# Kernel optimization log

Hardware: AMD Instinct MI355X
Metric: run time of the kernel (lower is better)

The kernel has to match this reference:

```python
import jax, jax.numpy as jnp
import numpy as np

WD = WH = WW = 7      # cubic window
NH = 3                # num_heads
RATE = 1              # idx == 1 -> rate = 1, num_heads_rate = 0
FF = 3.0              # focusing_factor (<= 6 branch)
EPS = 1e-6


def setup_inputs() -> dict:
    key = jax.random.key(0)
    ks = jax.random.split(key, 6)
    B, D, H, W, C = 1, 56, 56, 56, 96
    hd = C // NH
    x = jax.random.normal(ks[0], (B, D, H, W, C), dtype=jnp.float32)
    w_qkv = jax.random.normal(ks[1], (C, 3 * C), dtype=jnp.float32) * 0.02
    scale_param = jnp.zeros((RATE, 1, 1, hd), dtype=jnp.float32)
    pos_enc = jax.random.normal(ks[2], (RATE, 1, WD * WH * WW, hd), dtype=jnp.float32) * 0.02
    dwc_w = jax.random.normal(ks[3], (hd * RATE, 1, 5, 5, 5), dtype=jnp.float32) * 0.02
    dwc_b = jnp.zeros((hd * RATE,), dtype=jnp.float32)
    w_proj = jax.random.normal(ks[4], (C, C), dtype=jnp.float32) * 0.02
    b_proj = jnp.zeros((C,), dtype=jnp.float32)
    return {"x": x, "w_qkv": w_qkv, "scale_param": scale_param, "pos_enc": pos_enc,
            "dwc_w": dwc_w, "dwc_b": dwc_b, "w_proj": w_proj, "b_proj": b_proj}


def _forward(x, w_qkv, scale_param, pos_enc, dwc_w, dwc_b, w_proj, b_proj):
    B, D, H, W, C = x.shape
    hd = C // NH
    nD, nH_, nW_ = D // WD, H // WH, W // WW
    N = WD * WH * WW
    # qkv projection (no bias) -> (3, B, D, H, W, C)
    qkv = (x @ w_qkv).reshape(B, D, H, W, 3, C).transpose(4, 0, 1, 2, 3, 5)
    # window partition (rate == 1): (3, 1, B*nWin, N, C)
    qkv = qkv.reshape(3, B, nD, WD, nH_, WH, nW_, WW, C)
    qkv = qkv.transpose(0, 1, 2, 4, 6, 3, 5, 7, 8).reshape(3, RATE, B * nD * nH_ * nW_, N, C)
    q, k, v = qkv[0], qkv[1], qkv[2]

    def heads(t):  # 'r b n (h c) -> r (b h) n c'
        r, b, n, c0 = t.shape
        return t.reshape(r, b, n, NH, hd).transpose(0, 1, 3, 2, 4).reshape(r, b * NH, n, hd)

    q, k, v = heads(q), heads(k), heads(v)
    k = k + pos_enc
    scale = jax.nn.softplus(scale_param)
    q = (jax.nn.relu(q) + EPS) / scale
    k = (jax.nn.relu(k) + EPS) / scale
    qn = jnp.linalg.norm(q, axis=-1, keepdims=True)
    kn = jnp.linalg.norm(k, axis=-1, keepdims=True)
    q = q ** FF
    k = k ** FF
    q = q / jnp.linalg.norm(q, axis=-1, keepdims=True) * qn
    k = k / jnp.linalg.norm(k, axis=-1, keepdims=True) * kn
    # linear attention, kv-first branch (i*j*(c+d) > c*d*(i+j) for N=343, hd=32)
    z = 1.0 / (jnp.einsum('rbic,rbc->rbi', q, k.sum(axis=2)) + EPS)
    kv = jnp.einsum('rbjc,rbjd->rbcd', k, v)
    out = jnp.einsum('rbic,rbcd,rbi->rbid', q, kv, z)
    # depthwise 3D conv feature map on v: 'r b (d w h) c -> b (r c) d w h'
    r, b, n, c = v.shape
    fm = v.reshape(r, b, WD, WH, WW, c).transpose(1, 0, 5, 2, 3, 4).reshape(b, r * c, WD, WH, WW)
    fm = jax.lax.conv_general_dilated(fm, dwc_w, (1, 1, 1), [(2, 2)] * 3,
                                      dimension_numbers=('NCDHW', 'OIDHW', 'NCDHW'),
                                      feature_group_count=r * c)
    fm = fm + dwc_b[None, :, None, None, None]
    fm = fm.reshape(b, r, c, WD, WH, WW).transpose(1, 0, 3, 4, 5, 2).reshape(r, b, n, c)
    out = out + fm
    # merge heads: 'r (b h) n c -> r b n (h c)'
    Bw = b // NH
    out = out.reshape(r, Bw, NH, n, hd).transpose(0, 1, 3, 2, 4).reshape(r, Bw, n, C)
    # window reverse (rate == 1)
    out = out.reshape(B, nD, nH_, nW_, WD, WH, WW, C)
    out = out.transpose(0, 1, 4, 2, 5, 3, 6, 7).reshape(B, D, H, W, C)
    return out @ w_proj + b_proj


def reference(x, w_qkv, scale_param, pos_enc, dwc_w, dwc_b, w_proj, b_proj):
    return _forward(x, w_qkv, scale_param, pos_enc, dwc_w, dwc_b, w_proj, b_proj)
```

## Files before the change

### kernel.cpp

```cpp
#include <hip/hip_runtime.h>
#include <math.h>

#define NWIN 512
#define NHD  3
#define NTOK 343
#define HD   32
#define CH   96
#define DIM  56

#define XS 16.0f
#define WS 1024.0f
#define RS (1.0f/16384.0f)

typedef __attribute__((ext_vector_type(8))) _Float16 f16x8;
typedef __attribute__((ext_vector_type(4))) float f32x4;
typedef __attribute__((ext_vector_type(2))) _Float16 h2;

__device__ __forceinline__ unsigned short f2h_bits(float x) {
    _Float16 h = (_Float16)x;
    return __builtin_bit_cast(unsigned short, h);
}
__device__ __forceinline__ float h2f_bits(unsigned short u) {
    return (float)__builtin_bit_cast(_Float16, u);
}
__device__ __forceinline__ f32x4 mfma16h(f16x8 a, f16x8 b, f32x4 c) {
    return __builtin_amdgcn_mfma_f32_16x16x32_f16(a, b, c, 0, 0, 0);
}
__device__ __forceinline__ float shfl16_sum(float v) {
    v += __shfl_xor(v, 1);
    v += __shfl_xor(v, 2);
    v += __shfl_xor(v, 4);
    v += __shfl_xor(v, 8);
    return v;
}

__global__ void setup_w(const float* __restrict__ w_qkv,
                        unsigned short* __restrict__ wsb)
{
    int i = blockIdx.x * 256 + threadIdx.x;
    if (i >= 108 * 512) return;
    int e = i & 7, l = (i >> 3) & 63;
    int fid = i >> 9;
    int hl = fid & 1; int f2 = fid >> 1;
    int ks = f2 % 3; int f3 = f2 / 3;
    int nt = f3 & 1; int f4 = f3 >> 1;
    int m  = f4 % 3; int h  = f4 / 3;
    int kg  = ks * 32 + (l >> 4) * 8 + e;
    int col = m * 96 + h * 32 + nt * 16 + (l & 15);
    float w = w_qkv[kg * 288 + col] * WS;
    unsigned short hi = f2h_bits(w);
    wsb[i] = hl ? f2h_bits(w - h2f_bits(hi)) : hi;
}

#define BUILD_AFRAG(AH, AL, XPTR)                                           \
  { _Pragma("unroll")                                                       \
    for (int ks = 0; ks < 3; ++ks) {                                        \
        float4 x0 = *(const float4*)((XPTR) + ks * 32);                     \
        float4 x1 = *(const float4*)((XPTR) + ks * 32 + 4);                 \
        union { _Float16 e[8]; f16x8 v; } th, tl;                           \
        float s[8] = {x0.x, x0.y, x0.z, x0.w, x1.x, x1.y, x1.z, x1.w};      \
        _Pragma("unroll")                                                   \
        for (int e = 0; e < 8; ++e) {                                       \
            float sv = s[e] * XS;                                           \
            unsigned short hi = f2h_bits(sv);                               \
            th.e[e] = __builtin_bit_cast(_Float16, hi);                     \
            tl.e[e] = (_Float16)(sv - h2f_bits(hi));                       \
        }                                                                   \
        AH[ks] = th.v; AL[ks] = tl.v;                                       \
    } }

__global__ __launch_bounds__(256, 4) void attn_kernel(
    const float* __restrict__ x, const unsigned short* __restrict__ wsb,
    const float* __restrict__ scale_param, const float* __restrict__ pos_enc,
    const float* __restrict__ dwc_w, const float* __restrict__ dwc_b,
    float* __restrict__ y)
{
    __shared__ __align__(16) unsigned short v16[352 * HD];
    __shared__ __align__(16) union UU {
        struct PA { unsigned short kf16c[64 * 34]; } pa;
        struct PB {
            unsigned short qfL[64 * 40];
            unsigned short kvS[32 * 40];
            float ksred[4][2][16];
        } pb;
        unsigned dwcP[16 * 125];
        float pad_pin_lds[4000];
    } u;
    __shared__ float ksum_s[HD];
    __shared__ float sps[HD];

    const int tid = threadIdx.x, bid = blockIdx.x;
    const int swz = (bid & 7) * 192 + (bid >> 3);
    const int win = swz / 3;
    const int h   = swz - win * 3;
    const int wd = win >> 6, wh = (win >> 3) & 7, ww = win & 7;
    const int wv = tid >> 6, lane = tid & 63;
    const int quad = lane >> 4, li = lane & 15;
    const int mtw = wv >> 1, ntw = wv & 1;

    if (tid < HD) {
        float sv = scale_param[tid];
        sps[tid] = (sv > 20.f) ? sv : log1pf(expf(sv));
    }
    __syncthreads();
    const float sp0 = sps[li], sp1 = sps[16 + li];

    const f16x8* wf = (const f16x8*)wsb;
    const int fbase = h * 36;
    float ksp0 = 0.f, ksp1 = 0.f;
    f32x4 kvacc = {0.f, 0.f, 0.f, 0.f};

    for (int cb0 = 0; cb0 < NTOK; cb0 += 64) {
        const int nj = min(64, NTOK - cb0);
        int atok = cb0 + wv * 16 + li;
        int atc = min(atok, NTOK - 1);
        int adz = atc / 49, arem = atc - adz * 49, ady = arem / 7, adx = arem - ady * 7;
        int gA = ((wd * 7 + adz) * DIM + (wh * 7 + ady)) * DIM + (ww * 7 + adx);
        const float* xr = x + (size_t)gA * CH + quad * 8;
        f16x8 ah[3], al[3];
        BUILD_AFRAG(ah, al, xr);

        f32x4 ak[2] = {{0,0,0,0},{0,0,0,0}};
        f32x4 av[2] = {{0,0,0,0},{0,0,0,0}};
        #pragma unroll
        for (int nt = 0; nt < 2; ++nt) {
            #pragma unroll
            for (int ks = 0; ks < 3; ++ks) {
                int fk = (fbase + ((1 * 2 + nt) * 3 + ks) * 2) * 64 + lane;
                int fv = (fbase + ((2 * 2 + nt) * 3 + ks) * 2) * 64 + lane;
                f16x8 bkh = wf[fk], bkl = wf[fk + 64];
                f16x8 bvh = wf[fv];
                ak[nt] = mfma16h(ah[ks], bkh, ak[nt]);
                ak[nt] = mfma16h(ah[ks], bkl, ak[nt]);
                ak[nt] = mfma16h(al[ks], bkh, ak[nt]);
                av[nt] = mfma16h(ah[ks], bvh, av[nt]);
                av[nt] = mfma16h(al[ks], bvh, av[nt]);
            }
        }

        #pragma unroll
        for (int j = 0; j < 4; ++j) {
            int t16 = quad * 4 + j;
            int tok = cb0 + wv * 16 + t16;
            bool val = tok < NTOK;
            int tc = val ? tok : NTOK - 1;
            float pe0 = pos_enc[tc * HD + li];
            float pe1 = pos_enc[tc * HD + 16 + li];
            float kr0 = ak[0][j] * RS + pe0;
            float kr1 = ak[1][j] * RS + pe1;
            float kp0 = (fmaxf(kr0, 0.f) + 1e-6f) / sp0;
            float kp1 = (fmaxf(kr1, 0.f) + 1e-6f) / sp1;
            float k30 = kp0 * kp0 * kp0, k31 = kp1 * kp1 * kp1;
            float n2k = fmaf(kp0, kp0, kp1 * kp1);
            float n6k = fmaf(k30, k30, k31 * k31);
            n2k = shfl16_sum(n2k); n6k = shfl16_sum(n6k);
            float sk = sqrtf(n2k / n6k);
            float kf0 = k30 * sk, kf1 = k31 * sk;
            int tl = wv * 16 + t16;
            if (val) {
                ksp0 += kf0; ksp1 += kf1;
                u.pa.kf16c[tl * 34 + li]      = f2h_bits(kf0);
                u.pa.kf16c[tl * 34 + 16 + li] = f2h_bits(kf1);
                v16[tok * HD + li]      = f2h_bits(av[0][j] * RS);
                v16[tok * HD + 16 + li] = f2h_bits(av[1][j] * RS);
            } else {
                u.pa.kf16c[tl * 34 + li]      = 0;
                u.pa.kf16c[tl * 34 + 16 + li] = 0;
                if (tok < 352) {
                    v16[tok * HD + li]      = 0;
                    v16[tok * HD + 16 + li] = 0;
                }
            }
        }
        __syncthreads();

        const int nsteps = (nj + 31) >> 5;
        for (int s = 0; s < nsteps; ++s) {
            union { unsigned short u16a[8]; f16x8 v; } a8, b8;
            #pragma unroll
            for (int e = 0; e < 8; ++e) {
                int row = s * 32 + quad * 8 + e;
                a8.u16a[e] = u.pa.kf16c[row * 34 + mtw * 16 + li];
                b8.u16a[e] = v16[(cb0 + row) * HD + ntw * 16 + li];
            }
            kvacc = mfma16h(a8.v, b8.v, kvacc);
        }
        __syncthreads();
    }

    ksp0 += __shfl_xor(ksp0, 16); ksp0 += __shfl_xor(ksp0, 32);
    ksp1 += __shfl_xor(ksp1, 16); ksp1 += __shfl_xor(ksp1, 32);
    if (quad == 0) { u.pb.ksred[wv][0][li] = ksp0; u.pb.ksred[wv][1][li] = ksp1; }
    #pragma unroll
    for (int j = 0; j < 4; ++j)
        u.pb.kvS[(ntw * 16 + li) * 40 + mtw * 16 + quad * 4 + j] = f2h_bits(kvacc[j]);
    __syncthreads();
    if (tid < HD) {
        ksum_s[tid] = u.pb.ksred[0][tid >> 4][tid & 15] + u.pb.ksred[1][tid >> 4][tid & 15]
                    + u.pb.ksred[2][tid >> 4][tid & 15] + u.pb.ksred[3][tid >> 4][tid & 15];
    }
    __syncthreads();

    const float ks0 = ksum_s[li], ks1 = ksum_s[16 + li];
    for (int cb0 = 0; cb0 < NTOK; cb0 += 64) {
        int atok = cb0 + wv * 16 + li;
        int atc = min(atok, NTOK - 1);
        int adz = atc / 49, arem = atc - adz * 49, ady = arem / 7, adx = arem - ady * 7;
        int gA = ((wd * 7 + adz) * DIM + (wh * 7 + ady)) * DIM + (ww * 7 + adx);
        const float* xr = x + (size_t)gA * CH + quad * 8;
        f16x8 ah[3], al[3];
        BUILD_AFRAG(ah, al, xr);

        f32x4 aq[2] = {{0,0,0,0},{0,0,0,0}};
        #pragma unroll
        for (int nt = 0; nt < 2; ++nt) {
            #pragma unroll
            for (int ks = 0; ks < 3; ++ks) {
                int fq = (fbase + ((0 * 2 + nt) * 3 + ks) * 2) * 64 + lane;
                f16x8 bqh = wf[fq], bql = wf[fq + 64];
                aq[nt] = mfma16h(ah[ks], bqh, aq[nt]);
                aq[nt] = mfma16h(ah[ks], bql, aq[nt]);
                aq[nt] = mfma16h(al[ks], bqh, aq[nt]);
            }
        }

        float zq[4];
        #pragma unroll
        for (int j = 0; j < 4; ++j) {
            int t16 = quad * 4 + j;
            int tok = cb0 + wv * 16 + t16;
            bool val = tok < NTOK;
            float qp0 = (fmaxf(aq[0][j] * RS, 0.f) + 1e-6f) / sp0;
            float qp1 = (fmaxf(aq[1][j] * RS, 0.f) + 1e-6f) / sp1;
            float q30 = qp0 * qp0 * qp0, q31 = qp1 * qp1 * qp1;
            float n2q = fmaf(qp0, qp0, qp1 * qp1);
            float n6q = fmaf(q30, q30, q31 * q31);
            n2q = shfl16_sum(n2q); n6q = shfl16_sum(n6q);
            float sq = sqrtf(n2q / n6q);
            float qf0 = q30 * sq, qf1 = q31 * sq;
            float zp = shfl16_sum(fmaf(qf0, ks0, qf1 * ks1));
            zq[j] = 1.f / (zp + 1e-6f);
            if (val) {
                int tl = wv * 16 + t16;
                u.pb.qfL[tl * 40 + li]      = f2h_bits(qf0);
                u.pb.qfL[tl * 40 + 16 + li] = f2h_bits(qf1);
            }
        }
        f16x8 aqf = *(const f16x8*)&u.pb.qfL[(wv * 16 + li) * 40 + quad * 8];
        f16x8 bk0 = *(const f16x8*)&u.pb.kvS[li * 40 + quad * 8];
        f16x8 bk1 = *(const f16x8*)&u.pb.kvS[(16 + li) * 40 + quad * 8];
        f32x4 at0 = {0.f, 0.f, 0.f, 0.f}, at1 = {0.f, 0.f, 0.f, 0.f};
        at0 = mfma16h(aqf, bk0, at0);
        at1 = mfma16h(aqf, bk1, at1);

        #pragma unroll
        for (int j = 0; j < 4; ++j) {
            int t16 = quad * 4 + j;
            int tok = cb0 + wv * 16 + t16;
            if (tok < NTOK) {
                int dz = tok / 49, rem = tok - dz * 49, dy = rem / 7, dxx = rem - dy * 7;
                int g = ((wd * 7 + dz) * DIM + (wh * 7 + dy)) * DIM + (ww * 7 + dxx);
                y[(size_t)g * CH + h * HD + li]      = at0[j] * zq[j];
                y[(size_t)g * CH + h * HD + 16 + li] = at1[j] * zq[j];
            }
        }
    }

    __threadfence_block();
    __syncthreads();

    for (int i = tid; i < 16 * 125; i += 256) {
        int cp2 = i / 125, off = i - cp2 * 125;
        unsigned short a = f2h_bits(dwc_w[(2 * cp2) * 125 + off]);
        unsigned short b = f2h_bits(dwc_w[(2 * cp2 + 1) * 125 + off]);
        u.dwcP[i] = (unsigned)a | ((unsigned)b << 16);
    }
    __syncthreads();

    const int cp  = tid & 15;
    const int g16 = tid >> 4;
    const float bias0 = dwc_b[2 * cp], bias1 = dwc_b[2 * cp + 1];

    for (int it = g16; it < 49; it += 16) {
        int dz = it / 7, dy = it - dz * 7;
        h2 fm2[7] = {};
        #pragma unroll
        for (int ka2 = 0; ka2 < 5; ++ka2) {
            int za = dz + ka2 - 2;
            if ((unsigned)za >= 7u) continue;
            #pragma unroll
            for (int kb = 0; kb < 5; ++kb) {
                int zb = dy + kb - 2;
                if ((unsigned)zb >= 7u) continue;
                const unsigned* vb = (const unsigned*)&v16[(za * 49 + zb * 7) * HD + 2 * cp];
                h2 vr[7];
                #pragma unroll
                for (int xx = 0; xx < 7; ++xx)
                    vr[xx] = __builtin_bit_cast(h2, vb[xx * 16]);
                const unsigned* wb = &u.dwcP[cp * 125 + ka2 * 25 + kb * 5];
                h2 w0 = __builtin_bit_cast(h2, wb[0]);
                h2 w1 = __builtin_bit_cast(h2, wb[1]);
                h2 w2 = __builtin_bit_cast(h2, wb[2]);
                h2 w3 = __builtin_bit_cast(h2, wb[3]);
                h2 w4 = __builtin_bit_cast(h2, wb[4]);
                #pragma unroll
                for (int dx2 = 0; dx2 < 7; ++dx2) {
                    if (dx2 - 2 >= 0) fm2[dx2] += vr[dx2 - 2] * w0;
                    if (dx2 - 1 >= 0) fm2[dx2] += vr[dx2 - 1] * w1;
                    fm2[dx2] += vr[dx2] * w2;
                    if (dx2 + 1 <= 6) fm2[dx2] += vr[dx2 + 1] * w3;
                    if (dx2 + 2 <= 6) fm2[dx2] += vr[dx2 + 2] * w4;
                }
            }
        }
        int tokbase = ((wd * 7 + dz) * DIM + (wh * 7 + dy)) * DIM + ww * 7;
        #pragma unroll
        for (int dx2 = 0; dx2 < 7; ++dx2) {
            float* yp = &y[(size_t)(tokbase + dx2) * CH + h * HD + 2 * cp];
            float2 old = *(float2*)yp;
            old.x += (float)fm2[dx2][0] + bias0;
            old.y += (float)fm2[dx2][1] + bias1;
            *(float2*)yp = old;
        }
    }
}

__global__ __launch_bounds__(512, 1) void proj_kernel(
    const float* __restrict__ wp, const float* __restrict__ bp,
    float* __restrict__ y)
{
    __shared__ float yt[256 * 97];
    __shared__ float wl[96 * 96];

    const int tid = threadIdx.x;
    const int base = blockIdx.x * 256;

    for (int i = tid; i < 96 * 96; i += 512) wl[i] = wp[i];
    for (int i = tid; i < 256 * 96; i += 512) {
        int r = i / 96; int ch2 = i - r * 96;
        yt[r * 97 + ch2] = y[(base + r) * 96 + ch2];
    }
    __syncthreads();

    const int tokg = tid & 127;
    const int outg = tid >> 7;

    float acc[2][24];
    #pragma unroll
    for (int jj = 0; jj < 24; ++jj) {
        float b = bp[outg * 24 + jj];
        acc[0][jj] = b; acc[1][jj] = b;
    }

    for (int cc = 0; cc < 96; ++cc) {
        float y0 = yt[(tokg)       * 97 + cc];
        float y1 = yt[(tokg + 128) * 97 + cc];
        const float* wrow = &wl[cc * 96 + outg * 24];
        #pragma unroll
        for (int jj = 0; jj < 24; ++jj) {
            float wvv = wrow[jj];
            acc[0][jj] = fmaf(y0, wvv, acc[0][jj]);
            acc[1][jj] = fmaf(y1, wvv, acc[1][jj]);
        }
    }
    __syncthreads();

    #pragma unroll
    for (int i = 0; i < 2; ++i) {
        int tok = base + tokg + 128 * i;
        #pragma unroll
        for (int jj = 0; jj < 24; ++jj)
            y[tok * 96 + outg * 24 + jj] = acc[i][jj];
    }
}

extern "C" void kernel_launch(void* const* d_in, const int* in_sizes, int n_in,
                              void* d_out, int out_size, void* d_ws, size_t ws_size,
                              hipStream_t stream) {
    const float* x           = (const float*)d_in[0];
    const float* w_qkv       = (const float*)d_in[1];
    const float* scale_param = (const float*)d_in[2];
    const float* pos_enc     = (const float*)d_in[3];
    const float* dwc_w       = (const float*)d_in[4];
    const float* dwc_b       = (const float*)d_in[5];
    const float* w_proj      = (const float*)d_in[6];
    const float* b_proj      = (const float*)d_in[7];
    float* out = (float*)d_out;
    unsigned short* wsb = (unsigned short*)d_ws;

    setup_w<<<dim3(216), dim3(256), 0, stream>>>(w_qkv, wsb);
    attn_kernel<<<dim3(NHD * NWIN), dim3(256), 0, stream>>>(
        x, wsb, scale_param, pos_enc, dwc_w, dwc_b, out);
    proj_kernel<<<dim3(686), dim3(512), 0, stream>>>(w_proj, b_proj, out);
}
```

Baseline: 263.6 us.

## Compute Q in the first pass and keep it in LDS to avoid recomputing

The Q projection and its feature map are now computed in the first token pass, alongside K and V, from the same A fragments. The fp16 results are stored in a new LDS buffer covering all tokens. The second pass then reads Q from LDS instead of reloading x from global memory and redoing the split-fp16 conversion and the Q MFMAs. The cost is about 24 KB more LDS per block, so the occupancy hint in launch_bounds drops from 4 to 3 blocks per CU, and register pressure rises in the first pass.

```diff
diff --git a/kernel.cpp b/kernel.cpp
--- a/kernel.cpp
+++ b/kernel.cpp
@@ -64,28 +64,26 @@
             float sv = s[e] * XS;                                           \
             unsigned short hi = f2h_bits(sv);                               \
             th.e[e] = __builtin_bit_cast(_Float16, hi);                     \
-            tl.e[e] = (_Float16)(sv - h2f_bits(hi));                       \
+            tl.e[e] = (_Float16)(sv - h2f_bits(hi));                        \
         }                                                                   \
         AH[ks] = th.v; AL[ks] = tl.v;                                       \
     } }
 
-__global__ __launch_bounds__(256, 4) void attn_kernel(
+__global__ __launch_bounds__(256, 3) void attn_kernel(
     const float* __restrict__ x, const unsigned short* __restrict__ wsb,
     const float* __restrict__ scale_param, const float* __restrict__ pos_enc,
     const float* __restrict__ dwc_w, const float* __restrict__ dwc_b,
     float* __restrict__ y)
 {
     __shared__ __align__(16) unsigned short v16[352 * HD];
-    __shared__ __align__(16) union UU {
-        struct PA { unsigned short kf16c[64 * 34]; } pa;
-        struct PB {
-            unsigned short qfL[64 * 40];
-            unsigned short kvS[32 * 40];
-            float ksred[4][2][16];
-        } pb;
+    __shared__ __align__(16) union UQ {
+        unsigned short qf16[384 * 32];
         unsigned dwcP[16 * 125];
-        float pad_pin_lds[4000];
-    } u;
+    } uq;
+    __shared__ __align__(16) union UK {
+        unsigned short kf16c[64 * 34];
+        struct PB { unsigned short kvS[32 * 40]; float ksred[4][2][16]; } pb;
+    } uk;
     __shared__ float ksum_s[HD];
     __shared__ float sps[HD];
 
@@ -120,16 +118,22 @@
         f16x8 ah[3], al[3];
         BUILD_AFRAG(ah, al, xr);
 
+        f32x4 aq[2] = {{0,0,0,0},{0,0,0,0}};
         f32x4 ak[2] = {{0,0,0,0},{0,0,0,0}};
         f32x4 av[2] = {{0,0,0,0},{0,0,0,0}};
         #pragma unroll
         for (int nt = 0; nt < 2; ++nt) {
             #pragma unroll
             for (int ks = 0; ks < 3; ++ks) {
+                int fq = (fbase + ((0 * 2 + nt) * 3 + ks) * 2) * 64 + lane;
                 int fk = (fbase + ((1 * 2 + nt) * 3 + ks) * 2) * 64 + lane;
                 int fv = (fbase + ((2 * 2 + nt) * 3 + ks) * 2) * 64 + lane;
+                f16x8 bqh = wf[fq], bql = wf[fq + 64];
                 f16x8 bkh = wf[fk], bkl = wf[fk + 64];
                 f16x8 bvh = wf[fv];
+                aq[nt] = mfma16h(ah[ks], bqh, aq[nt]);
+                aq[nt] = mfma16h(ah[ks], bql, aq[nt]);
+                aq[nt] = mfma16h(al[ks], bqh, aq[nt]);
                 ak[nt] = mfma16h(ah[ks], bkh, ak[nt]);
                 ak[nt] = mfma16h(ah[ks], bkl, ak[nt]);
                 ak[nt] = mfma16h(al[ks], bkh, ak[nt]);
@@ -151,21 +155,30 @@
             float kp0 = (fmaxf(kr0, 0.f) + 1e-6f) / sp0;
             float kp1 = (fmaxf(kr1, 0.f) + 1e-6f) / sp1;
             float k30 = kp0 * kp0 * kp0, k31 = kp1 * kp1 * kp1;
+            float qp0 = (fmaxf(aq[0][j] * RS, 0.f) + 1e-6f) / sp0;
+            float qp1 = (fmaxf(aq[1][j] * RS, 0.f) + 1e-6f) / sp1;
+            float q30 = qp0 * qp0 * qp0, q31 = qp1 * qp1 * qp1;
             float n2k = fmaf(kp0, kp0, kp1 * kp1);
             float n6k = fmaf(k30, k30, k31 * k31);
+            float n2q = fmaf(qp0, qp0, qp1 * qp1);
+            float n6q = fmaf(q30, q30, q31 * q31);
             n2k = shfl16_sum(n2k); n6k = shfl16_sum(n6k);
-            float sk = sqrtf(n2k / n6k);
+            n2q = shfl16_sum(n2q); n6q = shfl16_sum(n6q);
+            float sk = sqrtf(n2k / n6k), sq = sqrtf(n2q / n6q);
             float kf0 = k30 * sk, kf1 = k31 * sk;
+            float qf0 = q30 * sq, qf1 = q31 * sq;
             int tl = wv * 16 + t16;
+            uq.qf16[tok * 32 + li]      = val ? f2h_bits(qf0) : (unsigned short)0;
+            uq.qf16[tok * 32 + 16 + li] = val ? f2h_bits(qf1) : (unsigned short)0;
             if (val) {
                 ksp0 += kf0; ksp1 += kf1;
-                u.pa.kf16c[tl * 34 + li]      = f2h_bits(kf0);
-                u.pa.kf16c[tl * 34 + 16 + li] = f2h_bits(kf1);
+                uk.kf16c[tl * 34 + li]      = f2h_bits(kf0);
+                uk.kf16c[tl * 34 + 16 + li] = f2h_bits(kf1);
                 v16[tok * HD + li]      = f2h_bits(av[0][j] * RS);
                 v16[tok * HD + 16 + li] = f2h_bits(av[1][j] * RS);
             } else {
-                u.pa.kf16c[tl * 34 + li]      = 0;
-                u.pa.kf16c[tl * 34 + 16 + li] = 0;
+                uk.kf16c[tl * 34 + li]      = 0;
+                uk.kf16c[tl * 34 + 16 + li] = 0;
                 if (tok < 352) {
                     v16[tok * HD + li]      = 0;
                     v16[tok * HD + 16 + li] = 0;
@@ -180,7 +193,7 @@
             #pragma unroll
             for (int e = 0; e < 8; ++e) {
                 int row = s * 32 + quad * 8 + e;
-                a8.u16a[e] = u.pa.kf16c[row * 34 + mtw * 16 + li];
+                a8.u16a[e] = uk.kf16c[row * 34 + mtw * 16 + li];
                 b8.u16a[e] = v16[(cb0 + row) * HD + ntw * 16 + li];
             }
             kvacc = mfma16h(a8.v, b8.v, kvacc);
@@ -190,73 +203,39 @@
 
     ksp0 += __shfl_xor(ksp0, 16); ksp0 += __shfl_xor(ksp0, 32);
     ksp1 += __shfl_xor(ksp1, 16); ksp1 += __shfl_xor(ksp1, 32);
-    if (quad == 0) { u.pb.ksred[wv][0][li] = ksp0; u.pb.ksred[wv][1][li] = ksp1; }
+    if (quad == 0) { uk.pb.ksred[wv][0][li] = ksp0; uk.pb.ksred[wv][1][li] = ksp1; }
     #pragma unroll
     for (int j = 0; j < 4; ++j)
-        u.pb.kvS[(ntw * 16 + li) * 40 + mtw * 16 + quad * 4 + j] = f2h_bits(kvacc[j]);
+        uk.pb.kvS[(ntw * 16 + li) * 40 + mtw * 16 + quad * 4 + j] = f2h_bits(kvacc[j]);
     __syncthreads();
     if (tid < HD) {
-        ksum_s[tid] = u.pb.ksred[0][tid >> 4][tid & 15] + u.pb.ksred[1][tid >> 4][tid & 15]
-                    + u.pb.ksred[2][tid >> 4][tid & 15] + u.pb.ksred[3][tid >> 4][tid & 15];
+        ksum_s[tid] = uk.pb.ksred[0][tid >> 4][tid & 15] + uk.pb.ksred[1][tid >> 4][tid & 15]
+                    + uk.pb.ksred[2][tid >> 4][tid & 15] + uk.pb.ksred[3][tid >> 4][tid & 15];
     }
     __syncthreads();
 
     const float ks0 = ksum_s[li], ks1 = ksum_s[16 + li];
     for (int cb0 = 0; cb0 < NTOK; cb0 += 64) {
-        int atok = cb0 + wv * 16 + li;
-        int atc = min(atok, NTOK - 1);
-        int adz = atc / 49, arem = atc - adz * 49, ady = arem / 7, adx = arem - ady * 7;
-        int gA = ((wd * 7 + adz) * DIM + (wh * 7 + ady)) * DIM + (ww * 7 + adx);
-        const float* xr = x + (size_t)gA * CH + quad * 8;
-        f16x8 ah[3], al[3];
-        BUILD_AFRAG(ah, al, xr);
-
-        f32x4 aq[2] = {{0,0,0,0},{0,0,0,0}};
-        #pragma unroll
-        for (int nt = 0; nt < 2; ++nt) {
-            #pragma unroll
-            for (int ks = 0; ks < 3; ++ks) {
-                int fq = (fbase + ((0 * 2 + nt) * 3 + ks) * 2) * 64 + lane;
-                f16x8 bqh = wf[fq], bql = wf[fq + 64];
-                aq[nt] = mfma16h(ah[ks], bqh, aq[nt]);
-                aq[nt] = mfma16h(ah[ks], bql, aq[nt]);
-                aq[nt] = mfma16h(al[ks], bqh, aq[nt]);
-            }
-        }
-
         float zq[4];
         #pragma unroll
         for (int j = 0; j < 4; ++j) {
-            int t16 = quad * 4 + j;
-            int tok = cb0 + wv * 16 + t16;
-            bool val = tok < NTOK;
-            float qp0 = (fmaxf(aq[0][j] * RS, 0.f) + 1e-6f) / sp0;
-            float qp1 = (fmaxf(aq[1][j] * RS, 0.f) + 1e-6f) / sp1;
-            float q30 = qp0 * qp0 * qp0, q31 = qp1 * qp1 * qp1;
-            float n2q = fmaf(qp0, qp0, qp1 * qp1);
-            float n6q = fmaf(q30, q30, q31 * q31);
-            n2q = shfl16_sum(n2q); n6q = shfl16_sum(n6q);
-            float sq = sqrtf(n2q / n6q);
-            float qf0 = q30 * sq, qf1 = q31 * sq;
+            int tok = cb0 + wv * 16 + quad * 4 + j;
+            int tc = min(tok, NTOK - 1);
+            float qf0 = h2f_bits(uq.qf16[tc * 32 + li]);
+            float qf1 = h2f_bits(uq.qf16[tc * 32 + 16 + li]);
             float zp = shfl16_sum(fmaf(qf0, ks0, qf1 * ks1));
             zq[j] = 1.f / (zp + 1e-6f);
-            if (val) {
-                int tl = wv * 16 + t16;
-                u.pb.qfL[tl * 40 + li]      = f2h_bits(qf0);
-                u.pb.qfL[tl * 40 + 16 + li] = f2h_bits(qf1);
-            }
-        }
-        f16x8 aqf = *(const f16x8*)&u.pb.qfL[(wv * 16 + li) * 40 + quad * 8];
-        f16x8 bk0 = *(const f16x8*)&u.pb.kvS[li * 40 + quad * 8];
-        f16x8 bk1 = *(const f16x8*)&u.pb.kvS[(16 + li) * 40 + quad * 8];
+        }
+        f16x8 aqf = *(const f16x8*)&uq.qf16[(cb0 + wv * 16 + li) * 32 + quad * 8];
+        f16x8 bk0 = *(const f16x8*)&uk.pb.kvS[li * 40 + quad * 8];
+        f16x8 bk1 = *(const f16x8*)&uk.pb.kvS[(16 + li) * 40 + quad * 8];
         f32x4 at0 = {0.f, 0.f, 0.f, 0.f}, at1 = {0.f, 0.f, 0.f, 0.f};
         at0 = mfma16h(aqf, bk0, at0);
         at1 = mfma16h(aqf, bk1, at1);
 
         #pragma unroll
         for (int j = 0; j < 4; ++j) {
-            int t16 = quad * 4 + j;
-            int tok = cb0 + wv * 16 + t16;
+            int tok = cb0 + wv * 16 + quad * 4 + j;
             if (tok < NTOK) {
                 int dz = tok / 49, rem = tok - dz * 49, dy = rem / 7, dxx = rem - dy * 7;
                 int g = ((wd * 7 + dz) * DIM + (wh * 7 + dy)) * DIM + (ww * 7 + dxx);
@@ -273,7 +252,7 @@
         int cp2 = i / 125, off = i - cp2 * 125;
         unsigned short a = f2h_bits(dwc_w[(2 * cp2) * 125 + off]);
         unsigned short b = f2h_bits(dwc_w[(2 * cp2 + 1) * 125 + off]);
-        u.dwcP[i] = (unsigned)a | ((unsigned)b << 16);
+        uq.dwcP[i] = (unsigned)a | ((unsigned)b << 16);
     }
     __syncthreads();
 
@@ -297,7 +276,7 @@
                 #pragma unroll
                 for (int xx = 0; xx < 7; ++xx)
                     vr[xx] = __builtin_bit_cast(h2, vb[xx * 16]);
-                const unsigned* wb = &u.dwcP[cp * 125 + ka2 * 25 + kb * 5];
+                const unsigned* wb = &uq.dwcP[cp * 125 + ka2 * 25 + kb * 5];
                 h2 w0 = __builtin_bit_cast(h2, wb[0]);
                 h2 w1 = __builtin_bit_cast(h2, wb[1]);
                 h2 w2 = __builtin_bit_cast(h2, wb[2]);
```

Result: slower. 274.8 us (+4.2%).

## Compute Q in the K/V pass and keep packed fp16 Q features in registers

Applied to the files above, without the earlier changes.

The Q projection and its focusing transform move into the first token loop, which already loads the x tile for K and V. The resulting fp16 Q features are kept in 24 packed registers per thread across the kv reduction, so the second pass no longer re-reads x from global memory or repeats the Q MFMAs. Both loops are fully unrolled and the kv B-fragments are loaded once. The cost is more register pressure from qreg and the extra live accumulators, which could lower occupancy or cause spills.

```diff
diff --git a/kernel.cpp b/kernel.cpp
--- a/kernel.cpp
+++ b/kernel.cpp
@@ -109,9 +109,12 @@
     const int fbase = h * 36;
     float ksp0 = 0.f, ksp1 = 0.f;
     f32x4 kvacc = {0.f, 0.f, 0.f, 0.f};
-
-    for (int cb0 = 0; cb0 < NTOK; cb0 += 64) {
-        const int nj = min(64, NTOK - cb0);
+    unsigned qreg[6][4];
+
+    #pragma unroll
+    for (int c6 = 0; c6 < 6; ++c6) {
+        const int cb0 = c6 * 64;
+        const int nj = (c6 < 5) ? 64 : (NTOK - 320);
         int atok = cb0 + wv * 16 + li;
         int atc = min(atok, NTOK - 1);
         int adz = atc / 49, arem = atc - adz * 49, ady = arem / 7, adx = arem - ady * 7;
@@ -120,16 +123,22 @@
         f16x8 ah[3], al[3];
         BUILD_AFRAG(ah, al, xr);
 
+        f32x4 aq[2] = {{0,0,0,0},{0,0,0,0}};
         f32x4 ak[2] = {{0,0,0,0},{0,0,0,0}};
         f32x4 av[2] = {{0,0,0,0},{0,0,0,0}};
         #pragma unroll
         for (int nt = 0; nt < 2; ++nt) {
             #pragma unroll
             for (int ks = 0; ks < 3; ++ks) {
+                int fq = (fbase + ((0 * 2 + nt) * 3 + ks) * 2) * 64 + lane;
                 int fk = (fbase + ((1 * 2 + nt) * 3 + ks) * 2) * 64 + lane;
                 int fv = (fbase + ((2 * 2 + nt) * 3 + ks) * 2) * 64 + lane;
+                f16x8 bqh = wf[fq], bql = wf[fq + 64];
                 f16x8 bkh = wf[fk], bkl = wf[fk + 64];
                 f16x8 bvh = wf[fv];
+                aq[nt] = mfma16h(ah[ks], bqh, aq[nt]);
+                aq[nt] = mfma16h(ah[ks], bql, aq[nt]);
+                aq[nt] = mfma16h(al[ks], bqh, aq[nt]);
                 ak[nt] = mfma16h(ah[ks], bkh, ak[nt]);
                 ak[nt] = mfma16h(ah[ks], bkl, ak[nt]);
                 ak[nt] = mfma16h(al[ks], bkh, ak[nt]);
@@ -151,11 +160,19 @@
             float kp0 = (fmaxf(kr0, 0.f) + 1e-6f) / sp0;
             float kp1 = (fmaxf(kr1, 0.f) + 1e-6f) / sp1;
             float k30 = kp0 * kp0 * kp0, k31 = kp1 * kp1 * kp1;
+            float qp0 = (fmaxf(aq[0][j] * RS, 0.f) + 1e-6f) / sp0;
+            float qp1 = (fmaxf(aq[1][j] * RS, 0.f) + 1e-6f) / sp1;
+            float q30 = qp0 * qp0 * qp0, q31 = qp1 * qp1 * qp1;
             float n2k = fmaf(kp0, kp0, kp1 * kp1);
             float n6k = fmaf(k30, k30, k31 * k31);
+            float n2q = fmaf(qp0, qp0, qp1 * qp1);
+            float n6q = fmaf(q30, q30, q31 * q31);
             n2k = shfl16_sum(n2k); n6k = shfl16_sum(n6k);
-            float sk = sqrtf(n2k / n6k);
+            n2q = shfl16_sum(n2q); n6q = shfl16_sum(n6q);
+            float sk = sqrtf(n2k / n6k), sq = sqrtf(n2q / n6q);
             float kf0 = k30 * sk, kf1 = k31 * sk;
+            float qf0 = q30 * sq, qf1 = q31 * sq;
+            qreg[c6][j] = (unsigned)f2h_bits(qf0) | ((unsigned)f2h_bits(qf1) << 16);
             int tl = wv * 16 + t16;
             if (val) {
                 ksp0 += kf0; ksp1 += kf1;
@@ -202,61 +219,31 @@
     __syncthreads();
 
     const float ks0 = ksum_s[li], ks1 = ksum_s[16 + li];
-    for (int cb0 = 0; cb0 < NTOK; cb0 += 64) {
-        int atok = cb0 + wv * 16 + li;
-        int atc = min(atok, NTOK - 1);
-        int adz = atc / 49, arem = atc - adz * 49, ady = arem / 7, adx = arem - ady * 7;
-        int gA = ((wd * 7 + adz) * DIM + (wh * 7 + ady)) * DIM + (ww * 7 + adx);
-        const float* xr = x + (size_t)gA * CH + quad * 8;
-        f16x8 ah[3], al[3];
-        BUILD_AFRAG(ah, al, xr);
-
-        f32x4 aq[2] = {{0,0,0,0},{0,0,0,0}};
-        #pragma unroll
-        for (int nt = 0; nt < 2; ++nt) {
-            #pragma unroll
-            for (int ks = 0; ks < 3; ++ks) {
-                int fq = (fbase + ((0 * 2 + nt) * 3 + ks) * 2) * 64 + lane;
-                f16x8 bqh = wf[fq], bql = wf[fq + 64];
-                aq[nt] = mfma16h(ah[ks], bqh, aq[nt]);
-                aq[nt] = mfma16h(ah[ks], bql, aq[nt]);
-                aq[nt] = mfma16h(al[ks], bqh, aq[nt]);
-            }
-        }
-
+    f16x8 bk0 = *(const f16x8*)&u.pb.kvS[li * 40 + quad * 8];
+    f16x8 bk1 = *(const f16x8*)&u.pb.kvS[(16 + li) * 40 + quad * 8];
+    #pragma unroll
+    for (int c6 = 0; c6 < 6; ++c6) {
+        const int cb0 = c6 * 64;
         float zq[4];
         #pragma unroll
         for (int j = 0; j < 4; ++j) {
-            int t16 = quad * 4 + j;
-            int tok = cb0 + wv * 16 + t16;
-            bool val = tok < NTOK;
-            float qp0 = (fmaxf(aq[0][j] * RS, 0.f) + 1e-6f) / sp0;
-            float qp1 = (fmaxf(aq[1][j] * RS, 0.f) + 1e-6f) / sp1;
-            float q30 = qp0 * qp0 * qp0, q31 = qp1 * qp1 * qp1;
-            float n2q = fmaf(qp0, qp0, qp1 * qp1);
-            float n6q = fmaf(q30, q30, q31 * q31);
-            n2q = shfl16_sum(n2q); n6q = shfl16_sum(n6q);
-            float sq = sqrtf(n2q / n6q);
-            float qf0 = q30 * sq, qf1 = q31 * sq;
+            unsigned qp = qreg[c6][j];
+            float qf0 = h2f_bits((unsigned short)(qp & 0xffff));
+            float qf1 = h2f_bits((unsigned short)(qp >> 16));
             float zp = shfl16_sum(fmaf(qf0, ks0, qf1 * ks1));
             zq[j] = 1.f / (zp + 1e-6f);
-            if (val) {
-                int tl = wv * 16 + t16;
-                u.pb.qfL[tl * 40 + li]      = f2h_bits(qf0);
-                u.pb.qfL[tl * 40 + 16 + li] = f2h_bits(qf1);
-            }
+            int tl = wv * 16 + quad * 4 + j;
+            u.pb.qfL[tl * 40 + li]      = (unsigned short)(qp & 0xffff);
+            u.pb.qfL[tl * 40 + 16 + li] = (unsigned short)(qp >> 16);
         }
         f16x8 aqf = *(const f16x8*)&u.pb.qfL[(wv * 16 + li) * 40 + quad * 8];
-        f16x8 bk0 = *(const f16x8*)&u.pb.kvS[li * 40 + quad * 8];
-        f16x8 bk1 = *(const f16x8*)&u.pb.kvS[(16 + li) * 40 + quad * 8];
         f32x4 at0 = {0.f, 0.f, 0.f, 0.f}, at1 = {0.f, 0.f, 0.f, 0.f};
         at0 = mfma16h(aqf, bk0, at0);
         at1 = mfma16h(aqf, bk1, at1);
 
         #pragma unroll
         for (int j = 0; j < 4; ++j) {
-            int t16 = quad * 4 + j;
-            int tok = cb0 + wv * 16 + t16;
+            int tok = cb0 + wv * 16 + quad * 4 + j;
             if (tok < NTOK) {
                 int dz = tok / 49, rem = tok - dz * 49, dy = rem / 7, dxx = rem - dy * 7;
                 int g = ((wd * 7 + dz) * DIM + (wh * 7 + dy)) * DIM + (ww * 7 + dxx);
```

After: 364.1 us. +38.1%, slower.
